# Kernel optimization log

Measured on AMD Instinct MI355X. Metric: run time of the kernel, lower is better.

## Reference

```python
import jax, jax.numpy as jnp
import numpy as np

T, B, E, H = 4096, 2, 1024, 16          # seq, batch, embed, heads
W = 256                                  # one-sided attention window (attention_window=512 // 2)
G = 64                                   # number of global tokens (first G positions)
D = E // H
NEG = -1e9


def _band_mask():
    # valid key position for band slot j at query t is t - W + j in [0, T)
    pos = jnp.arange(T)[:, None] - W + jnp.arange(2 * W + 1)[None, :]
    return (pos >= 0) & (pos < T)  # [T, 2W+1]


def _chunk_blocks(x):
    # x: [b, t, h, d] -> key/value blocks [b, nc, 3w, h, d]; block c covers positions [c*w - w, c*w + 2w)
    b, t, h, d = x.shape
    nc = t // W
    xp = jnp.pad(x, ((0, 0), (W, 2 * W), (0, 0), (0, 0)))
    idx = jnp.arange(nc)[:, None] * W + jnp.arange(3 * W)[None, :]
    return xp[:, idx]


def _band_qk(q, k):
    # q,k: [b,t,h,d] -> banded scores [b,t,h,2w+1] (Longformer sliding_chunks_matmul_qk)
    b, t, h, d = q.shape
    nc = t // W
    qc = q.reshape(b, nc, W, h, d)
    kb = _chunk_blocks(k)
    scores = jnp.einsum('bcxhd,bcyhd->bhcxy', qc, kb)          # y in [0, 3w)
    y_idx = jnp.arange(W)[:, None] + jnp.arange(2 * W + 1)[None, :]  # [w, 2w+1]
    band = jnp.take_along_axis(scores, y_idx[None, None, None], axis=-1)
    band = band.reshape(b, h, t, 2 * W + 1).transpose(0, 2, 1, 3)
    return jnp.where(_band_mask()[None, :, None, :], band, NEG)


def _band_pv(p, v):
    # p: [b,t,h,2w+1], v: [b,t,h,d] -> [b,t,h,d] (sliding_chunks_matmul_pv)
    b, t, h, _ = p.shape
    nc = t // W
    pb = p.transpose(0, 2, 1, 3).reshape(b, h, nc, W, 2 * W + 1)
    x = jnp.arange(W)
    y_idx = x[:, None] + jnp.arange(2 * W + 1)[None, :]
    p3 = jnp.zeros((b, h, nc, W, 3 * W), p.dtype).at[:, :, :, x[:, None], y_idx].set(pb)
    vb = _chunk_blocks(v)
    out = jnp.einsum('bhcxy,bcyhd->bcxhd', p3, vb)
    return out.reshape(b, t, h, -1)


def setup_inputs() -> dict:
    key = jax.random.key(0)
    ks = jax.random.split(key, 16)
    s = 0.02
    inp = {
        'query': jax.random.normal(ks[0], (T, B, E), jnp.float32),
        'attn_mask': jnp.concatenate([jnp.ones((B, G), jnp.int64), jnp.zeros((B, T - G), jnp.int64)], axis=1),
        'Wq': jax.random.normal(ks[1], (E, E), jnp.float32) * s, 'bq': jnp.zeros((E,), jnp.float32),
        'Wk': jax.random.normal(ks[2], (E, E), jnp.float32) * s, 'bk': jnp.zeros((E,), jnp.float32),
        'Wv': jax.random.normal(ks[3], (E, E), jnp.float32) * s, 'bv': jnp.zeros((E,), jnp.float32),
        'Wqg': jax.random.normal(ks[4], (E, E), jnp.float32) * s, 'bqg': jnp.zeros((E,), jnp.float32),
        'Wkg': jax.random.normal(ks[5], (E, E), jnp.float32) * s, 'bkg': jnp.zeros((E,), jnp.float32),
        'Wvg': jax.random.normal(ks[6], (E, E), jnp.float32) * s, 'bvg': jnp.zeros((E,), jnp.float32),
        'Wo': jax.random.normal(ks[7], (E, E), jnp.float32) * s, 'bo': jnp.zeros((E,), jnp.float32),
    }
    return inp


def reference(query, attn_mask, Wq, bq, Wk, bk, Wv, bv, Wqg, bqg, Wkg, bkg, Wvg, bvg, Wo, bo):
    del attn_mask  # structure fixed: first G tokens are global, no padding
    scaling = D ** -0.5
    x = query.transpose(1, 0, 2)                      # [b, t, e]
    q = ((x @ Wq.T + bq) * scaling).reshape(B, T, H, D)
    k = (x @ Wk.T + bk).reshape(B, T, H, D)
    v = (x @ Wv.T + bv).reshape(B, T, H, D)

    band = _band_qk(q, k)                             # [b,t,h,2w+1]
    sel_w = jnp.einsum('blhd,bshd->blhs', q, k[:, :G])  # every token attends global keys
    aw = jnp.concatenate([sel_w, band], axis=-1)
    probs = jax.nn.softmax(aw.astype(jnp.float32), axis=-1).astype(aw.dtype)

    attn = jnp.einsum('blhs,bshd->blhd', probs[..., :G], v[:, :G])
    attn = attn + _band_pv(probs[..., G:], v)         # [b,t,h,d]

    # global tokens attend everything with the *_global projections
    qg = ((x[:, :G] @ Wqg.T + bqg) * scaling).reshape(B, G, H, D)
    kg = (x @ Wkg.T + bkg).reshape(B, T, H, D)
    vg = (x @ Wvg.T + bvg).reshape(B, T, H, D)
    gs = jnp.einsum('bghd,bthd->bhgt', qg, kg)
    gp = jax.nn.softmax(gs.astype(jnp.float32), axis=-1).astype(gs.dtype)
    gout = jnp.einsum('bhgt,bthd->bghd', gp, vg)
    attn = attn.at[:, :G].set(gout)

    out = attn.reshape(B, T, E).transpose(1, 0, 2) @ Wo.T + bo  # [t, b, e]
    return out
```

## Files before the change

### kernel.cpp

```cpp
#include <hip/hip_runtime.h>
#include <hip/hip_bf16.h>

typedef unsigned short u16;
typedef __bf16 bf16x8 __attribute__((ext_vector_type(8)));
typedef float  f32x4  __attribute__((ext_vector_type(4)));

constexpr int TT = 4096;
constexpr int BBATCH = 2;
constexpr int EE = 1024;
constexpr int HH = 16;
constexpr int DD = 64;
constexpr int WQ = 256;
constexpr int GG = 64;
constexpr int NSPLIT = 8;

__device__ __forceinline__ u16 f2bf(float f) {
    union { float f; unsigned int i; } c; c.f = f;
    unsigned int x = c.i;
    return (u16)((x + 0x7fffu + ((x >> 16) & 1u)) >> 16);
}
__device__ __forceinline__ unsigned cvt_pk_bf16(float a, float b) {
    unsigned r;
    asm("v_cvt_pk_bf16_f32 %0, %1, %2" : "=v"(r) : "v"(a), "v"(b));
    return r;
}
__device__ __forceinline__ uint4 pack8(float4 a, float4 b) {
    uint4 r;
    r.x = (unsigned)f2bf(a.x) | ((unsigned)f2bf(a.y) << 16);
    r.y = (unsigned)f2bf(a.z) | ((unsigned)f2bf(a.w) << 16);
    r.z = (unsigned)f2bf(b.x) | ((unsigned)f2bf(b.y) << 16);
    r.w = (unsigned)f2bf(b.z) | ((unsigned)f2bf(b.w) << 16);
    return r;
}

__device__ __forceinline__ void g2l16(const u16* g, u16* l) {
    __builtin_amdgcn_global_load_lds(
        (const __attribute__((address_space(1))) void*)g,
        (__attribute__((address_space(3))) void*)l, 16, 0, 0);
}

__device__ __forceinline__ void xcd_swizzle(int& bx, int& by) {
    bx = blockIdx.x; by = blockIdx.y;
    if ((gridDim.y & 7) == 0) {
        const int g   = blockIdx.x + blockIdx.y * gridDim.x;
        const int idx = g >> 3;
        bx = idx % gridDim.x;
        by = (g & 7) + ((idx / gridDim.x) << 3);
    }
}

struct WPtrs { const float* p[7]; };
__global__ __launch_bounds__(256) void conv_kernel(
    WPtrs wp, const float* __restrict__ query, u16* __restrict__ wb, u16* __restrict__ xb)
{
    const size_t i8 = ((size_t)blockIdx.x * 256 + threadIdx.x) << 3;
    const size_t WTOT = (size_t)7 << 20;
    const float* src;
    u16* dst;
    if (i8 < WTOT) {
        const int which = (int)(i8 >> 20);
        src = wp.p[which] + (i8 & (((size_t)1 << 20) - 1));
        dst = wb + i8;
    } else {
        const size_t j = i8 - WTOT;
        const size_t e = j & (EE - 1);
        const size_t t = (j >> 10) & (TT - 1);
        const size_t b = j >> 22;
        src = query + (t * BBATCH + b) * EE + e;
        dst = xb + j;
    }
    const float4 f0 = *(const float4*)src;
    const float4 f1 = *(const float4*)(src + 4);
    *(uint4*)dst = pack8(f0, f1);
}

template<int C_F32, int PERMA_QG, int PERMC_TB>
__global__ __launch_bounds__(256) void gemm_kernel(
    const u16* __restrict__ A, const u16* __restrict__ W, const float* __restrict__ bias,
    void* __restrict__ Cv, float scale)
{
    const int tid = threadIdx.x, lane = tid & 63, w = tid >> 6;
    const int wm = w >> 1, wn = w & 1;
    int bx, by;
    xcd_swizzle(bx, by);
    const int m0 = by << 7, n0 = bx << 7;

    __shared__ __align__(16) u16 As[2 * 128 * 32];
    __shared__ __align__(16) u16 Bs[2 * 128 * 32];

    const int lrow = lane >> 2;
    const int lcol = (lane & 3) << 3;
    auto arow = [](int m) -> size_t {
        return PERMA_QG ? (size_t)(((m >> 6) << 12) | (m & 63)) : (size_t)m;
    };
    const u16* gA0 = A + arow(m0 + (w << 4) + lrow) * EE + lcol;
    const u16* gA1 = A + arow(m0 + 64 + (w << 4) + lrow) * EE + lcol;
    const u16* gB0 = W + (size_t)(n0 + (w << 4) + lrow) * EE + lcol;
    const u16* gB1 = gB0 + (size_t)64 * EE;
    u16* lA0 = As + (w << 9);
    u16* lA1 = As + 2048 + (w << 9);
    u16* lB0 = Bs + (w << 9);
    u16* lB1 = Bs + 2048 + (w << 9);

    f32x4 acc[4][4];
#pragma unroll
    for (int i = 0; i < 4; i++)
#pragma unroll
        for (int j = 0; j < 4; j++)
            acc[i][j] = (f32x4){0.f, 0.f, 0.f, 0.f};

    const int fr = lane & 15;
    const int fq = (lane >> 4) << 3;

    for (int k0 = 0; k0 < EE; k0 += 64) {
        g2l16(gA0 + k0, lA0);  g2l16(gA0 + k0 + 32, lA0 + 4096);
        g2l16(gA1 + k0, lA1);  g2l16(gA1 + k0 + 32, lA1 + 4096);
        g2l16(gB0 + k0, lB0);  g2l16(gB0 + k0 + 32, lB0 + 4096);
        g2l16(gB1 + k0, lB1);  g2l16(gB1 + k0 + 32, lB1 + 4096);
        __syncthreads();
#pragma unroll
        for (int p = 0; p < 2; p++) {
            bf16x8 af[4], bfv[4];
#pragma unroll
            for (int i = 0; i < 4; i++)
                af[i] = *(const bf16x8*)&As[p * 4096 + ((wm << 6) + (i << 4) + fr) * 32 + fq];
#pragma unroll
            for (int j = 0; j < 4; j++)
                bfv[j] = *(const bf16x8*)&Bs[p * 4096 + ((wn << 6) + (j << 4) + fr) * 32 + fq];
#pragma unroll
            for (int i = 0; i < 4; i++)
#pragma unroll
                for (int j = 0; j < 4; j++)
                    acc[i][j] = __builtin_amdgcn_mfma_f32_16x16x32_bf16(af[i], bfv[j], acc[i][j], 0, 0, 0);
        }
        __syncthreads();
    }

    const int colbase = n0 + (wn << 6);
    const int rowbase = m0 + (wm << 6) + ((lane >> 4) << 2);
#pragma unroll
    for (int j = 0; j < 4; j++) {
        const int col = colbase + (j << 4) + fr;
        const float bv = bias[col];
#pragma unroll
        for (int i = 0; i < 4; i++) {
#pragma unroll
            for (int r = 0; r < 4; r++) {
                const int row = rowbase + (i << 4) + r;
                const float val = (acc[i][j][r] + bv) * scale;
                const size_t dst = (size_t)(PERMC_TB ? (((row & (TT - 1)) << 1) | (row >> 12)) : row) * EE + col;
                if (C_F32) ((float*)Cv)[dst] = val;
                else       ((u16*)Cv)[dst]   = f2bf(val);
            }
        }
    }
}

struct FusedArgs { u16* out[3]; const float* bias[3]; float scale[3]; int vseg; };

template<int NSEG, int CF32, int PERMC>
__global__ __launch_bounds__(256, 2) void gemm_pipe_kernel(
    const u16* __restrict__ A, const u16* __restrict__ W, FusedArgs fa)
{
    const int tid = threadIdx.x, lane = tid & 63, w = tid >> 6;
    const int wm = w >> 1, wn = w & 1;
    int bx, by;
    xcd_swizzle(bx, by);
    const int m0 = by << 7, n0 = bx << 7;

    __shared__ __align__(16) u16 As[2][8192];
    __shared__ __align__(16) u16 Bs[2][8192];

    const int srow = lane >> 3;
    const int scol = ((lane & 7) ^ srow) << 3;
    const u16* gA = A + (size_t)(m0 + (w << 5) + srow) * EE + scol;
    const u16* gB = W + (size_t)(n0 + (w << 5) + srow) * EE + scol;
    u16* lA = &As[0][0] + (w << 11);
    u16* lB = &Bs[0][0] + (w << 11);

    f32x4 acc[4][4];
#pragma unroll
    for (int i = 0; i < 4; i++)
#pragma unroll
        for (int j = 0; j < 4; j++)
            acc[i][j] = (f32x4){0.f, 0.f, 0.f, 0.f};

    const int fr = lane & 15;
    const int qb = (lane >> 4) << 4;
    const int xr = (fr & 7) << 4;

    auto stageA = [&](int k0, int buf) {
#pragma unroll
        for (int l = 0; l < 4; l++)
            g2l16(gA + (size_t)(l << 3) * EE + k0, lA + buf * 8192 + (l << 9));
    };
    auto stageB = [&](int k0, int buf) {
#pragma unroll
        for (int l = 0; l < 4; l++)
            g2l16(gB + (size_t)(l << 3) * EE + k0, lB + buf * 8192 + (l << 9));
    };

    stageA(0, 0);
    stageB(0, 0);
    __syncthreads();

    constexpr int NT = EE / 64;
#pragma unroll 2
    for (int t = 0; t < NT; t++) {
        const int buf = t & 1;
        const bool pf = (t + 1 < NT);
        const int kn = (t + 1) << 6;
        bf16x8 af[4], bfv[4];

#pragma unroll
        for (int mi = 0; mi < 4; mi++)
            af[mi] = *(const bf16x8*)((const char*)&As[buf][0] +
                      ((((wm << 6) + (mi << 4) + fr)) << 7) + (qb ^ xr));
#pragma unroll
        for (int nj = 0; nj < 4; nj++)
            bfv[nj] = *(const bf16x8*)((const char*)&Bs[buf][0] +
                      ((((wn << 6) + (nj << 4) + fr)) << 7) + (qb ^ xr));
        if (pf) stageA(kn, buf ^ 1);
        __builtin_amdgcn_s_barrier();
        __builtin_amdgcn_s_setprio(1);
#pragma unroll
        for (int mi = 0; mi < 4; mi++)
#pragma unroll
            for (int nj = 0; nj < 4; nj++)
                acc[mi][nj] = __builtin_amdgcn_mfma_f32_16x16x32_bf16(af[mi], bfv[nj], acc[mi][nj], 0, 0, 0);
        __builtin_amdgcn_s_setprio(0);
        __builtin_amdgcn_s_barrier();

#pragma unroll
        for (int mi = 0; mi < 4; mi++)
            af[mi] = *(const bf16x8*)((const char*)&As[buf][0] +
                      ((((wm << 6) + (mi << 4) + fr)) << 7) + ((64 | qb) ^ xr));
#pragma unroll
        for (int nj = 0; nj < 4; nj++)
            bfv[nj] = *(const bf16x8*)((const char*)&Bs[buf][0] +
                      ((((wn << 6) + (nj << 4) + fr)) << 7) + ((64 | qb) ^ xr));
        if (pf) stageB(kn, buf ^ 1);
        __builtin_amdgcn_s_barrier();
        __builtin_amdgcn_s_setprio(1);
#pragma unroll
        for (int mi = 0; mi < 4; mi++)
#pragma unroll
            for (int nj = 0; nj < 4; nj++)
                acc[mi][nj] = __builtin_amdgcn_mfma_f32_16x16x32_bf16(af[mi], bfv[nj], acc[mi][nj], 0, 0, 0);
        __builtin_amdgcn_s_setprio(0);
        __syncthreads();
    }

    const int seg = (NSEG > 1) ? (n0 >> 10) : 0;
    u16* outp = fa.out[seg];
    const float* bp = fa.bias[seg];
    const float scl = fa.scale[seg];
    const bool vtr = (NSEG > 1) && (seg == fa.vseg);

    const int colbase = n0 + (wn << 6);
    const int rowbase = m0 + (wm << 6) + ((lane >> 4) << 2);
#pragma unroll
    for (int j = 0; j < 4; j++) {
        const int col = colbase + (j << 4) + fr;
        const int cl  = col & (EE - 1);
        const float bv = bp[cl];
#pragma unroll
        for (int i = 0; i < 4; i++) {
            if (vtr) {
                const int row0 = rowbase + (i << 4);
                const int bb = row0 >> 12, t = row0 & (TT - 1);
                const int hh = cl >> 6, d = cl & 63;
                ushort4 pk;
                pk.x = f2bf((acc[i][j][0] + bv) * scl);
                pk.y = f2bf((acc[i][j][1] + bv) * scl);
                pk.z = f2bf((acc[i][j][2] + bv) * scl);
                pk.w = f2bf((acc[i][j][3] + bv) * scl);
                *(ushort4*)(outp + (((size_t)(bb * HH + hh) * DD + d) * TT + t)) = pk;
            } else {
#pragma unroll
                for (int r = 0; r < 4; r++) {
                    const int row = rowbase + (i << 4) + r;
                    const float val = (acc[i][j][r] + bv) * scl;
                    const size_t drow = PERMC ? (size_t)(((row & (TT - 1)) << 1) | (row >> 12))
                                              : (size_t)row;
                    if (CF32) ((float*)outp)[drow * EE + cl] = val;
                    else      outp[drow * EE + cl] = f2bf(val);
                }
            }
        }
    }
}

__global__ __launch_bounds__(256) void band_attn_kernel(
    const u16* __restrict__ q, const u16* __restrict__ k, const u16* __restrict__ vt,
    u16* __restrict__ attnb)
{
    const int tid  = threadIdx.x;
    const int lane = tid & 63;
    const int w    = tid >> 6;
    const int col  = lane & 15;
    const int quad = lane >> 4;

    const int qt = blockIdx.x >> 5;
    const int bh = blockIdx.x & 31;
    const int h  = bh & (HH - 1);
    const int b  = bh >> 4;
    const int t0 = qt << 6;

    __shared__ __align__(16) u16 Ks[2][64][72];
    __shared__ __align__(16) u16 Vs[2][64][72];
    __shared__ __align__(16) u16 Ps[4][16][72];

    const size_t base   = (size_t)b * TT * EE + (size_t)h * DD;
    const size_t vtbase = (size_t)bh * DD * TT;

    const u16* qp = q + base + (size_t)(t0 + (w << 4) + col) * EE + (quad << 3);
    const bf16x8 qf0 = *(const bf16x8*)qp;
    const bf16x8 qf1 = *(const bf16x8*)(qp + 32);

    float m_i = -1e30f, l_i = 0.f;
    f32x4 acc_o[4];
#pragma unroll
    for (int nt = 0; nt < 4; nt++) acc_o[nt] = (f32x4){0.f, 0.f, 0.f, 0.f};

    const int c_lo = 1 + ((t0 < WQ) ? ((WQ - t0) >> 6) : 0);
    const int c_hi = min(9, 1 + ((TT + WQ - 64 - t0) >> 6));
    const int NTL  = 2 + c_hi - c_lo;

    const int srow  = tid >> 2;
    const int spart = (tid & 3) << 4;

    uint4 kr0, kr1, vr0, vr1;
    auto issue_loads = [&](int i) {
        const int kpos0 = (i == 0) ? 0 : (t0 - WQ + ((c_lo + i - 2) << 6));
        const u16* ks = k + base + (size_t)(kpos0 + srow) * EE + spart;
        const u16* vs = vt + vtbase + (size_t)srow * TT + kpos0 + spart;
        kr0 = *(const uint4*)ks;
        kr1 = *(const uint4*)(ks + 8);
        vr0 = *(const uint4*)vs;
        vr1 = *(const uint4*)(vs + 8);
    };
    auto write_stage = [&](int buf) {
        *(uint4*)&Ks[buf][srow][spart]     = kr0;
        *(uint4*)&Ks[buf][srow][spart + 8] = kr1;
        *(uint4*)&Vs[buf][srow][spart]     = vr0;
        *(uint4*)&Vs[buf][srow][spart + 8] = vr1;
    };

    issue_loads(0);
    write_stage(0);
    int buf = 0;

    const int qrow = (w << 4) + col;
    const int alsrc0 = (lane & 48) | ((lane >> 2) & 12);

#pragma unroll 1
    for (int i = 0; i < NTL; i++) {
        __syncthreads();
        const int c     = c_lo + i - 1;
        const int jbase = (i > 0 && (c == 1 || c == 9)) ? ((c - 1) << 6) : -1;
        const bool pf   = (i + 1 < NTL);
        if (pf) issue_loads(i + 1);

        f32x4 sT[4];
#pragma unroll
        for (int nt = 0; nt < 4; nt++) {
            const bf16x8 kf0 = *(const bf16x8*)&Ks[buf][(nt << 4) + col][quad << 3];
            const bf16x8 kf1 = *(const bf16x8*)&Ks[buf][(nt << 4) + col][32 + (quad << 3)];
            f32x4 s = (f32x4){0.f, 0.f, 0.f, 0.f};
            s = __builtin_amdgcn_mfma_f32_16x16x32_bf16(kf0, qf0, s, 0, 0, 0);
            s = __builtin_amdgcn_mfma_f32_16x16x32_bf16(kf1, qf1, s, 0, 0, 0);
            sT[nt] = s;
        }

        if (jbase >= 0) {
#pragma unroll
            for (int nt = 0; nt < 4; nt++) {
#pragma unroll
                for (int r = 0; r < 4; r++) {
                    const int jp = jbase + (nt << 4) + (quad << 2) + r;
                    const bool ok = (jp >= qrow) && (jp <= qrow + 2 * WQ);
                    if (!ok) sT[nt][r] = -1e30f;
                }
            }
        }

        float mx = sT[0][0];
#pragma unroll
        for (int nt = 0; nt < 4; nt++)
#pragma unroll
            for (int r = 0; r < 4; r++) mx = fmaxf(mx, sT[nt][r]);
        mx = fmaxf(mx, __shfl_xor(mx, 16));
        mx = fmaxf(mx, __shfl_xor(mx, 32));
        const float m_new = fmaxf(m_i, mx);
        const float alpha = __expf(m_i - m_new);
        m_i = m_new;
        l_i *= alpha;
        float ps = 0.f;
#pragma unroll
        for (int nt = 0; nt < 4; nt++)
#pragma unroll
            for (int r = 0; r < 4; r++) {
                const float e = __expf(sT[nt][r] - m_new);
                sT[nt][r] = e;
                ps += e;
            }
        ps += __shfl_xor(ps, 16);
        ps += __shfl_xor(ps, 32);
        l_i += ps;

        float al[4];
#pragma unroll
        for (int r = 0; r < 4; r++) al[r] = __shfl(alpha, alsrc0 | r);
#pragma unroll
        for (int nt = 0; nt < 4; nt++)
#pragma unroll
            for (int r = 0; r < 4; r++) acc_o[nt][r] *= al[r];

#pragma unroll
        for (int nt = 0; nt < 4; nt++) {
            uint2 pk2;
            pk2.x = cvt_pk_bf16(sT[nt][0], sT[nt][1]);
            pk2.y = cvt_pk_bf16(sT[nt][2], sT[nt][3]);
            *(uint2*)&Ps[w][col][(nt << 4) + (quad << 2)] = pk2;
        }

        const bf16x8 pf0 = *(const bf16x8*)&Ps[w][col][quad << 3];
        const bf16x8 pf1 = *(const bf16x8*)&Ps[w][col][32 + (quad << 3)];

#pragma unroll
        for (int nt = 0; nt < 4; nt++) {
            const bf16x8 vf0 = *(const bf16x8*)&Vs[buf][(nt << 4) + col][quad << 3];
            const bf16x8 vf1 = *(const bf16x8*)&Vs[buf][(nt << 4) + col][32 + (quad << 3)];
            acc_o[nt] = __builtin_amdgcn_mfma_f32_16x16x32_bf16(pf0, vf0, acc_o[nt], 0, 0, 0);
            acc_o[nt] = __builtin_amdgcn_mfma_f32_16x16x32_bf16(pf1, vf1, acc_o[nt], 0, 0, 0);
        }

        if (pf) write_stage(buf ^ 1);
        buf ^= 1;
    }

    float inv[4];
#pragma unroll
    for (int r = 0; r < 4; r++) inv[r] = 1.f / __shfl(l_i, alsrc0 | r);
#pragma unroll
    for (int nt = 0; nt < 4; nt++) {
#pragma unroll
        for (int r = 0; r < 4; r++) {
            const int t = t0 + (w << 4) + (quad << 2) + r;
            attnb[base + (size_t)t * EE + (nt << 4) + col] = f2bf(acc_o[nt][r] * inv[r]);
        }
    }
}

__global__ __launch_bounds__(256) void global_attn_flash_kernel(
    const u16* __restrict__ qg, const u16* __restrict__ kg, const u16* __restrict__ vg,
    float* __restrict__ Op, float* __restrict__ Ml, float* __restrict__ Ll)
{
    const int tid  = threadIdx.x;
    const int lane = tid & 63;
    const int w    = tid >> 6;
    const int col  = lane & 15;
    const int quad = lane >> 4;

    const int s  = blockIdx.x & (NSPLIT - 1);
    const int h  = (blockIdx.x >> 3) & (HH - 1);
    const int b  = blockIdx.x >> 7;
    const int k0pos = s * (TT / NSPLIT);

    __shared__ __align__(16) u16 Qs[64][72];
    __shared__ __align__(16) u16 Ks[64][72];
    __shared__ __align__(16) u16 Vs[64][70];
    __shared__ __align__(16) u16 Ps[4][16][72];

    const size_t base = (size_t)b * TT * EE + (size_t)h * DD;

    {
        const int qr   = tid >> 2;
        const int part = (tid & 3) << 4;
        const uint4* src = (const uint4*)(qg + (size_t)(b * GG + qr) * EE + (size_t)h * DD + part);
        *(uint4*)&Qs[qr][part]     = src[0];
        *(uint4*)&Qs[qr][part + 8] = src[1];
    }

    float m_i[4], l_i[4];
    f32x4 acc_o[4];
#pragma unroll
    for (int r = 0; r < 4; r++) { m_i[r] = -1e30f; l_i[r] = 0.f; }
#pragma unroll
    for (int nt = 0; nt < 4; nt++) acc_o[nt] = (f32x4){0.f, 0.f, 0.f, 0.f};

#pragma unroll 1
    for (int cc = 0; cc < TT / NSPLIT / 64; cc++) {
        {
            const int kk   = tid >> 2;
            const int part = (tid & 3) << 4;
            const int pos  = k0pos + (cc << 6) + kk;
            const uint4* ks = (const uint4*)(kg + base + (size_t)pos * EE + part);
            const uint4* vs = (const uint4*)(vg + base + (size_t)pos * EE + part);
            const uint4 k0v = ks[0], k1v = ks[1];
            const uint4 v0v = vs[0], v1v = vs[1];
            *(uint4*)&Ks[kk][part]     = k0v;
            *(uint4*)&Ks[kk][part + 8] = k1v;
            unsigned int* vd = (unsigned int*)&Vs[kk][part];
            vd[0] = v0v.x; vd[1] = v0v.y; vd[2] = v0v.z; vd[3] = v0v.w;
            vd[4] = v1v.x; vd[5] = v1v.y; vd[6] = v1v.z; vd[7] = v1v.w;
        }
        __syncthreads();

        bf16x8 qf0 = *(const bf16x8*)&Qs[(w << 4) + col][quad << 3];
        bf16x8 qf1 = *(const bf16x8*)&Qs[(w << 4) + col][32 + (quad << 3)];
        f32x4 acc_s[4];
#pragma unroll
        for (int nt = 0; nt < 4; nt++) {
            bf16x8 kf0 = *(const bf16x8*)&Ks[(nt << 4) + col][quad << 3];
            bf16x8 kf1 = *(const bf16x8*)&Ks[(nt << 4) + col][32 + (quad << 3)];
            f32x4 sv = (f32x4){0.f, 0.f, 0.f, 0.f};
            sv = __builtin_amdgcn_mfma_f32_16x16x32_bf16(qf0, kf0, sv, 0, 0, 0);
            sv = __builtin_amdgcn_mfma_f32_16x16x32_bf16(qf1, kf1, sv, 0, 0, 0);
            acc_s[nt] = sv;
        }

        float m_c[4], p_sum[4];
#pragma unroll
        for (int r = 0; r < 4; r++) {
            float mx = fmaxf(fmaxf(acc_s[0][r], acc_s[1][r]), fmaxf(acc_s[2][r], acc_s[3][r]));
#pragma unroll
            for (int off = 1; off < 16; off <<= 1) mx = fmaxf(mx, __shfl_xor(mx, off));
            m_c[r] = mx;
        }
#pragma unroll
        for (int r = 0; r < 4; r++) {
            const float m_new = fmaxf(m_i[r], m_c[r]);
            const float alpha = __expf(m_i[r] - m_new);
            m_i[r] = m_new;
            l_i[r] *= alpha;
#pragma unroll
            for (int nt = 0; nt < 4; nt++) acc_o[nt][r] *= alpha;
            float ps = 0.f;
#pragma unroll
            for (int nt = 0; nt < 4; nt++) {
                const float e = __expf(acc_s[nt][r] - m_new);
                acc_s[nt][r] = e;
                ps += e;
            }
            p_sum[r] = ps;
        }
#pragma unroll
        for (int r = 0; r < 4; r++) {
            float ps = p_sum[r];
#pragma unroll
            for (int off = 1; off < 16; off <<= 1) ps += __shfl_xor(ps, off);
            l_i[r] += ps;
        }

#pragma unroll
        for (int nt = 0; nt < 4; nt++)
#pragma unroll
            for (int r = 0; r < 4; r++)
                Ps[w][(quad << 2) + r][(nt << 4) + col] = f2bf(acc_s[nt][r]);

        bf16x8 pf0 = *(const bf16x8*)&Ps[w][col][quad << 3];
        bf16x8 pf1 = *(const bf16x8*)&Ps[w][col][32 + (quad << 3)];
#pragma unroll
        for (int nt = 0; nt < 4; nt++) {
            union { bf16x8 v; u16 e[8]; } vf0, vf1;
#pragma unroll
            for (int j = 0; j < 8; j++) {
                vf0.e[j] = Vs[(quad << 3) + j][(nt << 4) + col];
                vf1.e[j] = Vs[32 + (quad << 3) + j][(nt << 4) + col];
            }
            acc_o[nt] = __builtin_amdgcn_mfma_f32_16x16x32_bf16(pf0, vf0.v, acc_o[nt], 0, 0, 0);
            acc_o[nt] = __builtin_amdgcn_mfma_f32_16x16x32_bf16(pf1, vf1.v, acc_o[nt], 0, 0, 0);
        }
        __syncthreads();
    }

    const size_t obase = (size_t)blockIdx.x * GG * DD;
#pragma unroll
    for (int nt = 0; nt < 4; nt++) {
#pragma unroll
        for (int r = 0; r < 4; r++) {
            const int row = (w << 4) + (quad << 2) + r;
            Op[obase + (size_t)row * DD + (nt << 4) + col] = acc_o[nt][r];
        }
    }
    if (col == 0) {
#pragma unroll
        for (int r = 0; r < 4; r++) {
            const int row = (w << 4) + (quad << 2) + r;
            Ml[blockIdx.x * GG + row] = m_i[r];
            Ll[blockIdx.x * GG + row] = l_i[r];
        }
    }
}

__global__ __launch_bounds__(256) void global_combine_kernel(
    const float* __restrict__ Op, const float* __restrict__ Ml, const float* __restrict__ Ll,
    u16* __restrict__ attnb)
{
    const int bh  = blockIdx.x;
    const int b   = bh >> 4;
    const int h   = bh & (HH - 1);
    const int row = threadIdx.x >> 2;
    const int d0  = (threadIdx.x & 3) << 4;

    float mv[NSPLIT];
    float m = -1e30f;
#pragma unroll
    for (int s = 0; s < NSPLIT; s++) {
        mv[s] = Ml[(bh * NSPLIT + s) * GG + row];
        m = fmaxf(m, mv[s]);
    }
    float l = 0.f;
    float sc[NSPLIT];
#pragma unroll
    for (int s = 0; s < NSPLIT; s++) {
        sc[s] = __expf(mv[s] - m);
        l += Ll[(bh * NSPLIT + s) * GG + row] * sc[s];
    }
    float o[16];
#pragma unroll
    for (int j = 0; j < 16; j++) o[j] = 0.f;
#pragma unroll
    for (int s = 0; s < NSPLIT; s++) {
        const float* src = Op + ((size_t)(bh * NSPLIT + s) * GG + row) * DD + d0;
        const float f = sc[s];
#pragma unroll
        for (int j = 0; j < 16; j += 4) {
            const float4 v4 = *(const float4*)(src + j);
            o[j + 0] = fmaf(v4.x, f, o[j + 0]);
            o[j + 1] = fmaf(v4.y, f, o[j + 1]);
            o[j + 2] = fmaf(v4.z, f, o[j + 2]);
            o[j + 3] = fmaf(v4.w, f, o[j + 3]);
        }
    }
    const float inv = 1.f / l;
    u16* dst = attnb + ((size_t)b * TT + row) * EE + (size_t)h * DD + d0;
#pragma unroll
    for (int j = 0; j < 16; j++) dst[j] = f2bf(o[j] * inv);
}

extern "C" void kernel_launch(void* const* d_in, const int* in_sizes, int n_in,
                              void* d_out, int out_size, void* d_ws, size_t ws_size,
                              hipStream_t stream)
{
    (void)in_sizes; (void)n_in; (void)out_size; (void)ws_size;
    const float* query = (const float*)d_in[0];
    const float* Wq  = (const float*)d_in[2];  const float* bq  = (const float*)d_in[3];
    const float* Wk  = (const float*)d_in[4];  const float* bk  = (const float*)d_in[5];
    const float* Wv  = (const float*)d_in[6];  const float* bv  = (const float*)d_in[7];
    const float* Wqg = (const float*)d_in[8];  const float* bqg = (const float*)d_in[9];
    const float* Wkg = (const float*)d_in[10]; const float* bkg = (const float*)d_in[11];
    const float* Wvg = (const float*)d_in[12]; const float* bvg = (const float*)d_in[13];
    const float* Wo  = (const float*)d_in[14]; const float* bo  = (const float*)d_in[15];

    const size_t nfull = (size_t)BBATCH * TT * EE;
    const size_t wsz   = (size_t)1 << 20;
    u16* xb    = (u16*)d_ws;
    u16* wb    = xb + nfull;
    u16* slotA = wb + 7 * wsz;
    u16* slotB = slotA + nfull;
    u16* slotC = slotB + nfull;
    u16* qg    = slotC + nfull;
    float* Op  = (float*)(qg + (size_t)BBATCH * GG * EE);
    float* Ml  = Op + (size_t)BBATCH * HH * NSPLIT * GG * DD;
    float* Ll  = Ml + (size_t)BBATCH * HH * NSPLIT * GG;
    u16* attnb = xb;

    WPtrs wp;
    wp.p[0] = Wq; wp.p[1] = Wk; wp.p[2] = Wv;
    wp.p[3] = Wkg; wp.p[4] = Wvg; wp.p[5] = Wqg; wp.p[6] = Wo;

    const dim3 blk(256);
    const dim3 gF2(16, 64);
    const dim3 gF3(24, 64);
    const dim3 gFull(8, 64);
    const dim3 gQg(8, 1);
    const float sc = 0.125f;

    conv_kernel<<<7680, blk, 0, stream>>>(wp, query, wb, xb);

    gemm_kernel<0, 1, 0><<<gQg, blk, 0, stream>>>(xb, wb + 5 * wsz, bqg, qg, sc);

    FusedArgs fa2;
    fa2.out[0] = slotA; fa2.out[1] = slotB; fa2.out[2] = nullptr;
    fa2.bias[0] = bkg;  fa2.bias[1] = bvg;  fa2.bias[2] = nullptr;
    fa2.scale[0] = 1.f; fa2.scale[1] = 1.f; fa2.scale[2] = 1.f;
    fa2.vseg = -1;
    gemm_pipe_kernel<2, 0, 0><<<gF2, blk, 0, stream>>>(xb, wb + 3 * wsz, fa2);
    global_attn_flash_kernel<<<BBATCH * HH * NSPLIT, blk, 0, stream>>>(qg, slotA, slotB, Op, Ml, Ll);

    FusedArgs fa3;
    fa3.out[0] = slotA; fa3.out[1] = slotB; fa3.out[2] = slotC;
    fa3.bias[0] = bq;   fa3.bias[1] = bk;   fa3.bias[2] = bv;
    fa3.scale[0] = sc;  fa3.scale[1] = 1.f; fa3.scale[2] = 1.f;
    fa3.vseg = 2;
    gemm_pipe_kernel<3, 0, 0><<<gF3, blk, 0, stream>>>(xb, wb, fa3);

    band_attn_kernel<<<BBATCH * HH * (TT / 64), blk, 0, stream>>>(slotA, slotB, slotC, attnb);
    global_combine_kernel<<<BBATCH * HH, blk, 0, stream>>>(Op, Ml, Ll, attnb);

    FusedArgs faO;
    faO.out[0] = (u16*)d_out; faO.out[1] = nullptr; faO.out[2] = nullptr;
    faO.bias[0] = bo;         faO.bias[1] = nullptr; faO.bias[2] = nullptr;
    faO.scale[0] = 1.f;       faO.scale[1] = 1.f;    faO.scale[2] = 1.f;
    faO.vseg = -1;
    gemm_pipe_kernel<1, 1, 1><<<gFull, blk, 0, stream>>>(attnb, wb + 6 * wsz, faO);
}
```

Measured before the change: 343.1 us.

## Add 256x256-tile 512-thread GEMM for fused QKV and global KV projections

Adds a new GEMM kernel that computes 256x256 output tiles with 8 waves, double-buffered LDS staging and interleaved prefetch/MFMA phases with priority hints. The fused Q/K/V and global K/V projection launches switch to it with correspondingly smaller grids. Larger tiles are meant to raise operand reuse and cut global/LDS traffic per FLOP. In exchange it uses 128 KB of LDS per block and many accumulator registers, which may limit occupancy and leave fewer blocks than CUs for wave balance.

```diff
diff --git a/kernel.cpp b/kernel.cpp
--- a/kernel.cpp
+++ b/kernel.cpp
@@ -291,6 +291,160 @@
     }
 }
 
+template<int NSEG>
+__global__ __launch_bounds__(512, 2) void gemm_pipe256_kernel(
+    const u16* __restrict__ A, const u16* __restrict__ W, FusedArgs fa)
+{
+    const int tid = threadIdx.x, lane = tid & 63, w = tid >> 6;
+    const int wm = w >> 2, wn = w & 3;
+    int bx, by;
+    xcd_swizzle(bx, by);
+    const int m0 = by << 8, n0 = bx << 8;
+
+    __shared__ __align__(16) u16 As[2][16384];
+    __shared__ __align__(16) u16 Bs[2][16384];
+
+    const int srow = lane >> 3;
+    const int scol = ((lane & 7) ^ srow) << 3;
+    const u16* gA = A + (size_t)(m0 + (w << 5) + srow) * EE + scol;
+    const u16* gB = W + (size_t)(n0 + (w << 5) + srow) * EE + scol;
+    u16* lA = &As[0][0] + (w << 11);
+    u16* lB = &Bs[0][0] + (w << 11);
+
+    f32x4 acc[8][4];
+#pragma unroll
+    for (int i = 0; i < 8; i++)
+#pragma unroll
+        for (int j = 0; j < 4; j++)
+            acc[i][j] = (f32x4){0.f, 0.f, 0.f, 0.f};
+
+    const int fr = lane & 15;
+    const int qb = (lane >> 4) << 4;
+    const int xr = (fr & 7) << 4;
+
+    auto stageA = [&](int k0, int buf) {
+#pragma unroll
+        for (int l = 0; l < 4; l++)
+            g2l16(gA + (size_t)(l << 3) * EE + k0, lA + buf * 16384 + (l << 9));
+    };
+    auto stageB = [&](int k0, int buf) {
+#pragma unroll
+        for (int l = 0; l < 4; l++)
+            g2l16(gB + (size_t)(l << 3) * EE + k0, lB + buf * 16384 + (l << 9));
+    };
+
+    auto rdA = [&](int buf, int mh, int mi, int kh) -> bf16x8 {
+        const int row = (wm << 7) + (mh << 6) + (mi << 4) + fr;
+        return *(const bf16x8*)((const char*)&As[buf][0] + (row << 7) + (((kh << 6) | qb) ^ xr));
+    };
+    auto rdB = [&](int buf, int nj, int kh) -> bf16x8 {
+        const int row = (wn << 6) + (nj << 4) + fr;
+        return *(const bf16x8*)((const char*)&Bs[buf][0] + (row << 7) + (((kh << 6) | qb) ^ xr));
+    };
+
+    stageA(0, 0);
+    stageB(0, 0);
+    __syncthreads();
+
+    constexpr int NT = EE / 64;
+#pragma unroll 2
+    for (int t = 0; t < NT; t++) {
+        const int buf = t & 1;
+        const bool pf = (t + 1 < NT);
+        const int kn = (t + 1) << 6;
+        bf16x8 af[4], bfv[4];
+
+#pragma unroll
+        for (int mi = 0; mi < 4; mi++) af[mi] = rdA(buf, 0, mi, 0);
+#pragma unroll
+        for (int nj = 0; nj < 4; nj++) bfv[nj] = rdB(buf, nj, 0);
+        if (pf) stageA(kn, buf ^ 1);
+        __builtin_amdgcn_s_barrier();
+        __builtin_amdgcn_s_setprio(1);
+#pragma unroll
+        for (int mi = 0; mi < 4; mi++)
+#pragma unroll
+            for (int nj = 0; nj < 4; nj++)
+                acc[mi][nj] = __builtin_amdgcn_mfma_f32_16x16x32_bf16(af[mi], bfv[nj], acc[mi][nj], 0, 0, 0);
+        __builtin_amdgcn_s_setprio(0);
+        __builtin_amdgcn_s_barrier();
+
+#pragma unroll
+        for (int mi = 0; mi < 4; mi++) af[mi] = rdA(buf, 1, mi, 0);
+        if (pf) stageB(kn, buf ^ 1);
+        __builtin_amdgcn_s_barrier();
+        __builtin_amdgcn_s_setprio(1);
+#pragma unroll
+        for (int mi = 0; mi < 4; mi++)
+#pragma unroll
+            for (int nj = 0; nj < 4; nj++)
+                acc[4 + mi][nj] = __builtin_amdgcn_mfma_f32_16x16x32_bf16(af[mi], bfv[nj], acc[4 + mi][nj], 0, 0, 0);
+        __builtin_amdgcn_s_setprio(0);
+        __builtin_amdgcn_s_barrier();
+
+#pragma unroll
+        for (int mi = 0; mi < 4; mi++) af[mi] = rdA(buf, 0, mi, 1);
+#pragma unroll
+        for (int nj = 0; nj < 4; nj++) bfv[nj] = rdB(buf, nj, 1);
+        __builtin_amdgcn_s_barrier();
+        __builtin_amdgcn_s_setprio(1);
+#pragma unroll
+        for (int mi = 0; mi < 4; mi++)
+#pragma unroll
+            for (int nj = 0; nj < 4; nj++)
+                acc[mi][nj] = __builtin_amdgcn_mfma_f32_16x16x32_bf16(af[mi], bfv[nj], acc[mi][nj], 0, 0, 0);
+        __builtin_amdgcn_s_setprio(0);
+        __builtin_amdgcn_s_barrier();
+
+#pragma unroll
+        for (int mi = 0; mi < 4; mi++) af[mi] = rdA(buf, 1, mi, 1);
+        __builtin_amdgcn_s_barrier();
+        __builtin_amdgcn_s_setprio(1);
+#pragma unroll
+        for (int mi = 0; mi < 4; mi++)
+#pragma unroll
+            for (int nj = 0; nj < 4; nj++)
+                acc[4 + mi][nj] = __builtin_amdgcn_mfma_f32_16x16x32_bf16(af[mi], bfv[nj], acc[4 + mi][nj], 0, 0, 0);
+        __builtin_amdgcn_s_setprio(0);
+        __syncthreads();
+    }
+
+    const int seg = (NSEG > 1) ? (n0 >> 10) : 0;
+    u16* outp = fa.out[seg];
+    const float* bp = fa.bias[seg];
+    const float scl = fa.scale[seg];
+    const bool vtr = (NSEG > 1) && (seg == fa.vseg);
+
+    const int colbase = n0 + (wn << 6);
+    const int rowbase = m0 + (wm << 7) + ((lane >> 4) << 2);
+#pragma unroll
+    for (int j = 0; j < 4; j++) {
+        const int col = colbase + (j << 4) + fr;
+        const int cl  = col & (EE - 1);
+        const float bv = bp[cl];
+#pragma unroll
+        for (int i = 0; i < 8; i++) {
+            if (vtr) {
+                const int row0 = rowbase + (i << 4);
+                const int bb = row0 >> 12, t = row0 & (TT - 1);
+                const int hh = cl >> 6, d = cl & 63;
+                ushort4 pk;
+                pk.x = f2bf((acc[i][j][0] + bv) * scl);
+                pk.y = f2bf((acc[i][j][1] + bv) * scl);
+                pk.z = f2bf((acc[i][j][2] + bv) * scl);
+                pk.w = f2bf((acc[i][j][3] + bv) * scl);
+                *(ushort4*)(outp + (((size_t)(bb * HH + hh) * DD + d) * TT + t)) = pk;
+            } else {
+#pragma unroll
+                for (int r = 0; r < 4; r++) {
+                    const int row = rowbase + (i << 4) + r;
+                    outp[(size_t)row * EE + cl] = f2bf((acc[i][j][r] + bv) * scl);
+                }
+            }
+        }
+    }
+}
+
 __global__ __launch_bounds__(256) void band_attn_kernel(
     const u16* __restrict__ q, const u16* __restrict__ k, const u16* __restrict__ vt,
     u16* __restrict__ attnb)
@@ -673,8 +827,9 @@
     wp.p[3] = Wkg; wp.p[4] = Wvg; wp.p[5] = Wqg; wp.p[6] = Wo;
 
     const dim3 blk(256);
-    const dim3 gF2(16, 64);
-    const dim3 gF3(24, 64);
+    const dim3 blk512(512);
+    const dim3 gF2(8, 32);
+    const dim3 gF3(12, 32);
     const dim3 gFull(8, 64);
     const dim3 gQg(8, 1);
     const float sc = 0.125f;
@@ -688,7 +843,7 @@
     fa2.bias[0] = bkg;  fa2.bias[1] = bvg;  fa2.bias[2] = nullptr;
     fa2.scale[0] = 1.f; fa2.scale[1] = 1.f; fa2.scale[2] = 1.f;
     fa2.vseg = -1;
-    gemm_pipe_kernel<2, 0, 0><<<gF2, blk, 0, stream>>>(xb, wb + 3 * wsz, fa2);
+    gemm_pipe256_kernel<2><<<gF2, blk512, 0, stream>>>(xb, wb + 3 * wsz, fa2);
     global_attn_flash_kernel<<<BBATCH * HH * NSPLIT, blk, 0, stream>>>(qg, slotA, slotB, Op, Ml, Ll);
 
     FusedArgs fa3;
@@ -696,7 +851,7 @@
     fa3.bias[0] = bq;   fa3.bias[1] = bk;   fa3.bias[2] = bv;
     fa3.scale[0] = sc;  fa3.scale[1] = 1.f; fa3.scale[2] = 1.f;
     fa3.vseg = 2;
-    gemm_pipe_kernel<3, 0, 0><<<gF3, blk, 0, stream>>>(xb, wb, fa3);
+    gemm_pipe256_kernel<3><<<gF3, blk512, 0, stream>>>(xb, wb, fa3);
 
     band_attn_kernel<<<BBATCH * HH * (TT / 64), blk, 0, stream>>>(slotA, slotB, slotC, attnb);
     global_combine_kernel<<<BBATCH * HH, blk, 0, stream>>>(Op, Ml, Ll, attnb);
```

Result: slower. 367.7 us (+7.2%).

## Restructure global flash attention with transposed V, double buffering, and row-per-lane softmax

Applied to the files above, without the earlier changes.

The global-token flash kernel now reads V from a transposed layout produced by the K/V projection GEMM (vseg=1), so V fragments load as vectors instead of scalar strided LDS reads. K/V tiles are double-buffered in shared memory, with the next tile's global loads issued before the current tile's compute, and Q fragments come straight from global memory into registers. The S tile is computed transposed so each lane owns one query row, which reduces the softmax reductions to two shuffles. P is packed into LDS with cvt_pk_bf16. The kernel depends on the GEMM emitting the transposed V layout correctly and uses more LDS.

```diff
diff --git a/kernel.cpp b/kernel.cpp
--- a/kernel.cpp
+++ b/kernel.cpp
@@ -454,7 +454,7 @@
 }
 
 __global__ __launch_bounds__(256) void global_attn_flash_kernel(
-    const u16* __restrict__ qg, const u16* __restrict__ kg, const u16* __restrict__ vg,
+    const u16* __restrict__ qg, const u16* __restrict__ kg, const u16* __restrict__ vgt,
     float* __restrict__ Op, float* __restrict__ Ml, float* __restrict__ Ll)
 {
     const int tid  = threadIdx.x;
@@ -468,112 +468,119 @@
     const int b  = blockIdx.x >> 7;
     const int k0pos = s * (TT / NSPLIT);
 
-    __shared__ __align__(16) u16 Qs[64][72];
-    __shared__ __align__(16) u16 Ks[64][72];
-    __shared__ __align__(16) u16 Vs[64][70];
+    __shared__ __align__(16) u16 Ks[2][64][72];
+    __shared__ __align__(16) u16 Vs[2][64][72];
     __shared__ __align__(16) u16 Ps[4][16][72];
 
-    const size_t base = (size_t)b * TT * EE + (size_t)h * DD;
-
-    {
-        const int qr   = tid >> 2;
-        const int part = (tid & 3) << 4;
-        const uint4* src = (const uint4*)(qg + (size_t)(b * GG + qr) * EE + (size_t)h * DD + part);
-        *(uint4*)&Qs[qr][part]     = src[0];
-        *(uint4*)&Qs[qr][part + 8] = src[1];
-    }
-
-    float m_i[4], l_i[4];
+    const size_t base   = (size_t)b * TT * EE + (size_t)h * DD;
+    const size_t vtbase = (size_t)((b << 4) | h) * DD * TT;
+
+    const u16* qp = qg + (size_t)(b * GG + (w << 4) + col) * EE + (size_t)h * DD + (quad << 3);
+    const bf16x8 qf0 = *(const bf16x8*)qp;
+    const bf16x8 qf1 = *(const bf16x8*)(qp + 32);
+
+    float m_i = -1e30f, l_i = 0.f;
     f32x4 acc_o[4];
 #pragma unroll
-    for (int r = 0; r < 4; r++) { m_i[r] = -1e30f; l_i[r] = 0.f; }
-#pragma unroll
     for (int nt = 0; nt < 4; nt++) acc_o[nt] = (f32x4){0.f, 0.f, 0.f, 0.f};
 
+    constexpr int NTL = TT / NSPLIT / 64;
+    const int srow  = tid >> 2;
+    const int spart = (tid & 3) << 4;
+
+    uint4 kr0, kr1, vr0, vr1;
+    auto issue_loads = [&](int i) {
+        const int kpos0 = k0pos + (i << 6);
+        const u16* ks = kg + base + (size_t)(kpos0 + srow) * EE + spart;
+        const u16* vs = vgt + vtbase + (size_t)srow * TT + kpos0 + spart;
+        kr0 = *(const uint4*)ks;
+        kr1 = *(const uint4*)(ks + 8);
+        vr0 = *(const uint4*)vs;
+        vr1 = *(const uint4*)(vs + 8);
+    };
+    auto write_stage = [&](int buf) {
+        *(uint4*)&Ks[buf][srow][spart]     = kr0;
+        *(uint4*)&Ks[buf][srow][spart + 8] = kr1;
+        *(uint4*)&Vs[buf][srow][spart]     = vr0;
+        *(uint4*)&Vs[buf][srow][spart + 8] = vr1;
+    };
+
+    issue_loads(0);
+    write_stage(0);
+    int buf = 0;
+
+    const int alsrc0 = (lane & 48) | ((lane >> 2) & 12);
+
 #pragma unroll 1
-    for (int cc = 0; cc < TT / NSPLIT / 64; cc++) {
-        {
-            const int kk   = tid >> 2;
-            const int part = (tid & 3) << 4;
-            const int pos  = k0pos + (cc << 6) + kk;
-            const uint4* ks = (const uint4*)(kg + base + (size_t)pos * EE + part);
-            const uint4* vs = (const uint4*)(vg + base + (size_t)pos * EE + part);
-            const uint4 k0v = ks[0], k1v = ks[1];
-            const uint4 v0v = vs[0], v1v = vs[1];
-            *(uint4*)&Ks[kk][part]     = k0v;
-            *(uint4*)&Ks[kk][part + 8] = k1v;
-            unsigned int* vd = (unsigned int*)&Vs[kk][part];
-            vd[0] = v0v.x; vd[1] = v0v.y; vd[2] = v0v.z; vd[3] = v0v.w;
-            vd[4] = v1v.x; vd[5] = v1v.y; vd[6] = v1v.z; vd[7] = v1v.w;
-        }
+    for (int i = 0; i < NTL; i++) {
         __syncthreads();
-
-        bf16x8 qf0 = *(const bf16x8*)&Qs[(w << 4) + col][quad << 3];
-        bf16x8 qf1 = *(const bf16x8*)&Qs[(w << 4) + col][32 + (quad << 3)];
-        f32x4 acc_s[4];
+        const bool pf = (i + 1 < NTL);
+        if (pf) issue_loads(i + 1);
+
+        f32x4 sT[4];
 #pragma unroll
         for (int nt = 0; nt < 4; nt++) {
-            bf16x8 kf0 = *(const bf16x8*)&Ks[(nt << 4) + col][quad << 3];
-            bf16x8 kf1 = *(const bf16x8*)&Ks[(nt << 4) + col][32 + (quad << 3)];
+            const bf16x8 kf0 = *(const bf16x8*)&Ks[buf][(nt << 4) + col][quad << 3];
+            const bf16x8 kf1 = *(const bf16x8*)&Ks[buf][(nt << 4) + col][32 + (quad << 3)];
             f32x4 sv = (f32x4){0.f, 0.f, 0.f, 0.f};
-            sv = __builtin_amdgcn_mfma_f32_16x16x32_bf16(qf0, kf0, sv, 0, 0, 0);
-            sv = __builtin_amdgcn_mfma_f32_16x16x32_bf16(qf1, kf1, sv, 0, 0, 0);
-            acc_s[nt] = sv;
-        }
-
-        float m_c[4], p_sum[4];
-#pragma unroll
-        for (int r = 0; r < 4; r++) {
-            float mx = fmaxf(fmaxf(acc_s[0][r], acc_s[1][r]), fmaxf(acc_s[2][r], acc_s[3][r]));
-#pragma unroll
-            for (int off = 1; off < 16; off <<= 1) mx = fmaxf(mx, __shfl_xor(mx, off));
-            m_c[r] = mx;
-        }
-#pragma unroll
-        for (int r = 0; r < 4; r++) {
-            const float m_new = fmaxf(m_i[r], m_c[r]);
-            const float alpha = __expf(m_i[r] - m_new);
-            m_i[r] = m_new;
-            l_i[r] *= alpha;
-#pragma unroll
-            for (int nt = 0; nt < 4; nt++) acc_o[nt][r] *= alpha;
-            float ps = 0.f;
-#pragma unroll
-            for (int nt = 0; nt < 4; nt++) {
-                const float e = __expf(acc_s[nt][r] - m_new);
-                acc_s[nt][r] = e;
+            sv = __builtin_amdgcn_mfma_f32_16x16x32_bf16(kf0, qf0, sv, 0, 0, 0);
+            sv = __builtin_amdgcn_mfma_f32_16x16x32_bf16(kf1, qf1, sv, 0, 0, 0);
+            sT[nt] = sv;
+        }
+
+        float mx = sT[0][0];
+#pragma unroll
+        for (int nt = 0; nt < 4; nt++)
+#pragma unroll
+            for (int r = 0; r < 4; r++) mx = fmaxf(mx, sT[nt][r]);
+        mx = fmaxf(mx, __shfl_xor(mx, 16));
+        mx = fmaxf(mx, __shfl_xor(mx, 32));
+        const float m_new = fmaxf(m_i, mx);
+        const float alpha = __expf(m_i - m_new);
+        m_i = m_new;
+        l_i *= alpha;
+        float ps = 0.f;
+#pragma unroll
+        for (int nt = 0; nt < 4; nt++)
+#pragma unroll
+            for (int r = 0; r < 4; r++) {
+                const float e = __expf(sT[nt][r] - m_new);
+                sT[nt][r] = e;
                 ps += e;
             }
-            p_sum[r] = ps;
-        }
-#pragma unroll
-        for (int r = 0; r < 4; r++) {
-            float ps = p_sum[r];
-#pragma unroll
-            for (int off = 1; off < 16; off <<= 1) ps += __shfl_xor(ps, off);
-            l_i[r] += ps;
-        }
-
+        ps += __shfl_xor(ps, 16);
+        ps += __shfl_xor(ps, 32);
+        l_i += ps;
+
+        float al[4];
+#pragma unroll
+        for (int r = 0; r < 4; r++) al[r] = __shfl(alpha, alsrc0 | r);
 #pragma unroll
         for (int nt = 0; nt < 4; nt++)
 #pragma unroll
-            for (int r = 0; r < 4; r++)
-                Ps[w][(quad << 2) + r][(nt << 4) + col] = f2bf(acc_s[nt][r]);
-
-        bf16x8 pf0 = *(const bf16x8*)&Ps[w][col][quad << 3];
-        bf16x8 pf1 = *(const bf16x8*)&Ps[w][col][32 + (quad << 3)];
+            for (int r = 0; r < 4; r++) acc_o[nt][r] *= al[r];
+
 #pragma unroll
         for (int nt = 0; nt < 4; nt++) {
-            union { bf16x8 v; u16 e[8]; } vf0, vf1;
-#pragma unroll
-            for (int j = 0; j < 8; j++) {
-                vf0.e[j] = Vs[(quad << 3) + j][(nt << 4) + col];
-                vf1.e[j] = Vs[32 + (quad << 3) + j][(nt << 4) + col];
-            }
-            acc_o[nt] = __builtin_amdgcn_mfma_f32_16x16x32_bf16(pf0, vf0.v, acc_o[nt], 0, 0, 0);
-            acc_o[nt] = __builtin_amdgcn_mfma_f32_16x16x32_bf16(pf1, vf1.v, acc_o[nt], 0, 0, 0);
-        }
-        __syncthreads();
+            uint2 pk2;
+            pk2.x = cvt_pk_bf16(sT[nt][0], sT[nt][1]);
+            pk2.y = cvt_pk_bf16(sT[nt][2], sT[nt][3]);
+            *(uint2*)&Ps[w][col][(nt << 4) + (quad << 2)] = pk2;
+        }
+
+        const bf16x8 pf0 = *(const bf16x8*)&Ps[w][col][quad << 3];
+        const bf16x8 pf1 = *(const bf16x8*)&Ps[w][col][32 + (quad << 3)];
+
+#pragma unroll
+        for (int nt = 0; nt < 4; nt++) {
+            const bf16x8 vf0 = *(const bf16x8*)&Vs[buf][(nt << 4) + col][quad << 3];
+            const bf16x8 vf1 = *(const bf16x8*)&Vs[buf][(nt << 4) + col][32 + (quad << 3)];
+            acc_o[nt] = __builtin_amdgcn_mfma_f32_16x16x32_bf16(pf0, vf0, acc_o[nt], 0, 0, 0);
+            acc_o[nt] = __builtin_amdgcn_mfma_f32_16x16x32_bf16(pf1, vf1, acc_o[nt], 0, 0, 0);
+        }
+
+        if (pf) write_stage(buf ^ 1);
+        buf ^= 1;
     }
 
     const size_t obase = (size_t)blockIdx.x * GG * DD;
@@ -585,13 +592,9 @@
             Op[obase + (size_t)row * DD + (nt << 4) + col] = acc_o[nt][r];
         }
     }
-    if (col == 0) {
-#pragma unroll
-        for (int r = 0; r < 4; r++) {
-            const int row = (w << 4) + (quad << 2) + r;
-            Ml[blockIdx.x * GG + row] = m_i[r];
-            Ll[blockIdx.x * GG + row] = l_i[r];
-        }
+    if (quad == 0) {
+        Ml[blockIdx.x * GG + (w << 4) + col] = m_i;
+        Ll[blockIdx.x * GG + (w << 4) + col] = l_i;
     }
 }
 
@@ -687,7 +690,7 @@
     fa2.out[0] = slotA; fa2.out[1] = slotB; fa2.out[2] = nullptr;
     fa2.bias[0] = bkg;  fa2.bias[1] = bvg;  fa2.bias[2] = nullptr;
     fa2.scale[0] = 1.f; fa2.scale[1] = 1.f; fa2.scale[2] = 1.f;
-    fa2.vseg = -1;
+    fa2.vseg = 1;
     gemm_pipe_kernel<2, 0, 0><<<gF2, blk, 0, stream>>>(xb, wb + 3 * wsz, fa2);
     global_attn_flash_kernel<<<BBATCH * HH * NSPLIT, blk, 0, stream>>>(qg, slotA, slotB, Op, Ml, Ll);
 
```

New measurement: 341.4 us. Within noise of the previous version (-0.5%).
